# Kernel optimization log

Hardware: AMD Instinct MI355X
Metric: run time of the kernel (lower is better)

## Reference

```python
import jax, jax.numpy as jnp
import numpy as np

DIM = 512
HEADS = 8
DIM_HEAD = 64
INNER = HEADS * DIM_HEAD  # 512
PATCH = 64
M = 3
IN_CH = PATCH * PATCH // 2      # 2048
OUT_CH = IN_CH // 2             # 1024
B, N = 8, PATCH * PATCH // 4    # 8, 1024
SCALE = DIM_HEAD ** -0.5


def setup_inputs() -> dict:
    key = jax.random.key(0)
    ks = jax.random.split(key, 16)
    rn = lambda k, shp, s: (jax.random.normal(k, shp, dtype=jnp.float32) * s)
    inp = rn(ks[0], (B, N, DIM), 1.0)
    x = rn(ks[1], (B, N, DIM), 1.0)
    y = rn(ks[2], (B, N, DIM), 1.0)
    # Linear params (torch convention: W [out, in], y = x @ W.T + b)
    Wq = rn(ks[3], (INNER, DIM), DIM ** -0.5)
    bq = jnp.zeros((INNER,), jnp.float32)
    Wkv = rn(ks[4], (2 * INNER, DIM), DIM ** -0.5)
    bkv = jnp.zeros((2 * INNER,), jnp.float32)
    Wf = rn(ks[5], (OUT_CH + M, IN_CH + M), (IN_CH + M) ** -0.5)
    bf = jnp.zeros((OUT_CH + M,), jnp.float32)
    Wo = rn(ks[6], (DIM, INNER), INNER ** -0.5)
    bo = jnp.zeros((DIM,), jnp.float32)
    # memory tokens (xavier_normal std = sqrt(2/(m+inner)))
    std = np.sqrt(2.0 / (M + INNER))
    m_k = rn(ks[7], (1, M, INNER), std)
    m_v = rn(ks[8], (1, M, INNER), std)
    Sm_k = rn(ks[9], (1, M, INNER), std)
    Sm_v = rn(ks[10], (1, M, INNER), std)
    return dict(inp=inp, x=x, y=y, Wq=Wq, bq=bq, Wkv=Wkv, bkv=bkv,
                Wf=Wf, bf=bf, Wo=Wo, bo=bo,
                m_k=m_k, m_v=m_v, Sm_k=Sm_k, Sm_v=Sm_v)


def _split_heads(t):
    # 'b n (h d) -> b h n d'
    b, n, _ = t.shape
    return t.reshape(b, n, HEADS, DIM_HEAD).transpose(0, 2, 1, 3)


def _mem_view(p, b):
    # torch: p.expand(b, M, INNER).view(b, HEADS, M, DIM_HEAD) — raw reshape
    return jnp.broadcast_to(p, (b, M, INNER)).reshape(b, HEADS, M, DIM_HEAD)


def reference(inp, x, y, Wq, bq, Wkv, bkv, Wf, bf, Wo, bo, m_k, m_v, Sm_k, Sm_v):
    b = inp.shape[0]
    context = jnp.concatenate([x, y], axis=1)            # [b, 2n, dim]
    q = _split_heads(inp @ Wq.T + bq)                    # [b, h, n, d]
    kv = context @ Wkv.T + bkv
    k, v = jnp.split(kv, 2, axis=-1)
    k, v = _split_heads(k), _split_heads(v)              # [b, h, 2n, d]
    mk = np.sqrt(DIM_HEAD).astype(np.float32) * _mem_view(m_k, b)
    mv = np.sqrt(M).astype(np.float32) * _mem_view(m_v, b)
    k = jnp.concatenate([k, mk], axis=2)                 # [b, h, 2n+m, d]
    v = jnp.concatenate([v, mv], axis=2)
    dots = jnp.einsum('bhid,bhjd->bhij', q, k) * SCALE
    cross_attn = jax.nn.softmax(dots, axis=-1)           # [b, h, n, 2n+m]

    skv = inp @ Wkv.T + bkv
    S_k, S_v = jnp.split(skv, 2, axis=-1)
    S_k, S_v = _split_heads(S_k), _split_heads(S_v)      # [b, h, n, d]
    Smk = np.sqrt(DIM_HEAD).astype(np.float32) * _mem_view(Sm_k, b)
    Smv = np.sqrt(M).astype(np.float32) * _mem_view(Sm_v, b)
    Sk = jnp.concatenate([S_k, Smk], axis=2)             # [b, h, n+m, d]
    Sv = jnp.concatenate([S_v, Smv], axis=2)
    dots2 = jnp.einsum('bhid,bhjd->bhij', q, Sk) * SCALE
    self_attn = jax.nn.softmax(dots2, axis=-1)           # [b, h, n, n+m]

    cross_attn = cross_attn @ Wf.T + bf                  # [b, h, n, n+m]
    attn = cross_attn + self_attn
    out = jnp.einsum('bhij,bhjd->bhid', attn, Sv)        # [b, h, n, d]
    out = out.transpose(0, 2, 1, 3).reshape(b, -1, INNER)
    return out @ Wo.T + bo                               # [b, n, dim]
```

## Files before the change

### kernel.cpp

```cpp
#include <hip/hip_runtime.h>
#include <hip/hip_bf16.h>
#include <type_traits>

using bf16 = __hip_bfloat16;
typedef float f32x4 __attribute__((ext_vector_type(4)));
typedef __bf16 bf16x8_t __attribute__((ext_vector_type(8)));
typedef short  s16x8_t  __attribute__((ext_vector_type(8)));

template <typename V, typename = void> struct MfmaWorks : std::false_type {};
template <typename V>
struct MfmaWorks<V, std::void_t<decltype(__builtin_amdgcn_mfma_f32_16x16x32_bf16(
    std::declval<V>(), std::declval<V>(), std::declval<f32x4>(), 0, 0, 0))>> : std::true_type {};
using frag_t = std::conditional_t<MfmaWorks<bf16x8_t>::value, bf16x8_t, s16x8_t>;

template <typename V>
__device__ __forceinline__ f32x4 mfma_16x16x32(V a, V b, f32x4 c) {
    return __builtin_amdgcn_mfma_f32_16x16x32_bf16(a, b, c, 0, 0, 0);
}

__device__ __forceinline__ void gld_lds16(const void* g, void* l) {
    __builtin_amdgcn_global_load_lds(
        (const __attribute__((address_space(1))) unsigned int*)g,
        (__attribute__((address_space(3))) unsigned int*)l, 16, 0, 0);
}

__device__ __forceinline__ unsigned pack2(float lo, float hi) {
    bf16 a = __float2bfloat16(lo), b = __float2bfloat16(hi);
    unsigned short al, bl;
    __builtin_memcpy(&al, &a, 2);
    __builtin_memcpy(&bl, &b, 2);
    return (unsigned)al | ((unsigned)bl << 16);
}

__device__ __forceinline__ float ldin(const void* p, long i, int f32) {
    return f32 ? ((const float*)p)[i] : __bfloat162float(((const bf16*)p)[i]);
}

__global__ void detect_dtype(const void* __restrict__ inp, int* __restrict__ flag)
{
    const int t = threadIdx.x;
    int sane_cnt = 0;
#pragma unroll
    for (int s = 0; s < 4; s++) {
        float v = __bfloat162float(((const bf16*)inp)[2 * (t + 64 * s)]);
        float a = fabsf(v);
        bool sane = (a == 0.f) || (a > 9e-4f && a < 1000.f);
        unsigned long long m = __ballot(sane);
        sane_cnt += (int)__popcll(m);
    }
    if (t == 0) *flag = (sane_cnt > 128) ? 0 : 1;
}

__global__ __launch_bounds__(256)
void cvt_gen8(const void* __restrict__ src, bf16* __restrict__ dst,
              long ndst, const int* __restrict__ flag, float scale)
{
    const int f = *flag;
    const long i0 = ((long)blockIdx.x * 256 + threadIdx.x) * 8;
    if (i0 >= ndst) return;
#pragma unroll
    for (int u = 0; u < 8; u++)
        dst[i0 + u] = __float2bfloat16(scale * ldin(src, i0 + u, f));
}

__global__ __launch_bounds__(256)
void prep(const void* __restrict__ Wq, const void* __restrict__ Wkv,
          const void* __restrict__ Wo, const void* __restrict__ Wf,
          const void* __restrict__ bff, const void* __restrict__ bq,
          const void* __restrict__ bkv, const void* __restrict__ bo,
          const void* __restrict__ mk, const void* __restrict__ Smk,
          const void* __restrict__ Smv,
          bf16* __restrict__ WqB, bf16* __restrict__ WkvB, bf16* __restrict__ WoB,
          bf16* __restrict__ WfT, bf16* __restrict__ bqB, bf16* __restrict__ bkvB,
          bf16* __restrict__ boB, bf16* __restrict__ kb, bf16* __restrict__ Skb,
          bf16* __restrict__ GTS, bf16* __restrict__ SvC,
          const int* __restrict__ flag, float qscale)
{
    const int f = *flag;
    const int blk = blockIdx.x;
    const int t = threadIdx.x;
    const float SQRT3 = 1.7320508f;

    if (blk < 512) {
        long id = (long)blk * 256 + t;
        const void* src; bf16* dst; float sc;
        if (blk < 128)      { src = Wq;  dst = WqB;  sc = qscale; }
        else if (blk < 384) { src = Wkv; dst = WkvB; sc = 1.f; id -= 128L * 256; }
        else                { src = Wo;  dst = WoB;  sc = 1.f; id -= 384L * 256; }
        const long i0 = id * 8;
#pragma unroll
        for (int u = 0; u < 8; u++)
            dst[i0 + u] = __float2bfloat16(sc * ldin(src, i0 + u, f));
    } else if (blk < 1634) {
        const long i0 = ((long)(blk - 512) * 256 + t) * 8;
        if (i0 >= 2176L * 1056) return;
        const long j = i0 / 1056, r0 = i0 % 1056;
        __align__(16) bf16 tmp[8];
#pragma unroll
        for (int u = 0; u < 8; u++) {
            const long r = r0 + u;
            float v = 0.f;
            if (r < 1027) {
                if (j < 2051)       v = ldin(Wf, r * 2051 + j, f);
                else if (j == 2051) v = ldin(bff, r, f);
            }
            tmp[u] = __float2bfloat16(v);
        }
        *(uint4*)(WfT + i0) = *(const uint4*)tmp;
    } else if (blk < 1637) {
        const void* src; bf16* dst; int n; float sc;
        switch (blk - 1634) {
            case 0:  src = bq;  dst = bqB;  n = 512;  sc = qscale; break;
            case 1:  src = bkv; dst = bkvB; n = 1024; sc = 1.f;    break;
            default: src = bo;  dst = boB;  n = 512;  sc = 1.f;    break;
        }
        for (int i = t; i < n; i += 256)
            dst[i] = __float2bfloat16(sc * ldin(src, i, f));
    } else if (blk < 1893) {
        const long e = ((long)(blk - 1637) * 256 + t) * 8;
        const long bh = e >> 13, rem = e & 8191;
        const long jj = rem >> 6, dg0 = rem & 63;
        const long h = bh & 7;
        __align__(16) bf16 tmp[8];
#pragma unroll
        for (int u = 0; u < 8; u++) {
            float v = (jj < 3) ? 8.f * ldin(mk, jj * 512 + h * 64 + dg0 + u, f) : 0.f;
            tmp[u] = __float2bfloat16(v);
        }
        *(uint4*)(kb + (bh * 2176 + 2048 + jj) * 64 + dg0) = *(const uint4*)tmp;
    } else if (blk < 2149) {
        const long e = ((long)(blk - 1893) * 256 + t) * 8;
        const long bh = e >> 13, rem = e & 8191;
        const long jj = rem >> 6, dg0 = rem & 63;
        const long h = bh & 7;
        __align__(16) bf16 tmp[8];
#pragma unroll
        for (int u = 0; u < 8; u++) {
            float v = (jj < 3) ? 8.f * ldin(Smk, jj * 512 + h * 64 + dg0 + u, f) : 0.f;
            tmp[u] = __float2bfloat16(v);
        }
        *(uint4*)(Skb + (bh * 1152 + 1024 + jj) * 64 + dg0) = *(const uint4*)tmp;
    } else {
        const long e = ((long)(blk - 2149) * 256 + t) * 8;
        const long bh = e >> 11, rem = e & 2047;
        const long dd = rem >> 5, jc0 = rem & 31;
        const long h = bh & 7;
        __align__(16) bf16 tmp[8];
#pragma unroll
        for (int u = 0; u < 8; u++) {
            const long jc = jc0 + u;
            float v = (jc < 3) ? SQRT3 * ldin(Smv, jc * 512 + h * 64 + dd, f) : 0.f;
            tmp[u] = __float2bfloat16(v);
        }
        *(uint4*)(GTS + (bh * 128 + dd) * 3136 + 3104 + jc0) = *(const uint4*)tmp;
        *(uint4*)(SvC + (bh * 64 + dd) * 1056 + 1024 + jc0)  = *(const uint4*)tmp;
    }
}

__global__ __launch_bounds__(256)
void cvt_ctx8(const void* __restrict__ x, const void* __restrict__ y,
              bf16* __restrict__ ctx, const int* __restrict__ flag)
{
    const int f = *flag;
    const long i0 = ((long)blockIdx.x * 256 + threadIdx.x) * 8;
    const long r = i0 >> 9, c0 = i0 & 511;
    const long b = r >> 11, jj = r & 2047;
    const void* src = (jj < 1024) ? x : y;
    const long  soff = (jj < 1024) ? ((b * 1024 + jj) * 512 + c0)
                                   : ((b * 1024 + (jj - 1024)) * 512 + c0);
#pragma unroll
    for (int u = 0; u < 8; u++)
        ctx[i0 + u] = __float2bfloat16(ldin(src, soff + u, f));
}

#define TM 128
#define TN 128
#define BK 32

template<int OMODE>
__global__ __launch_bounds__(256)
void gemm_nt(const bf16* __restrict__ A, long lda, long sAz,
             const bf16* __restrict__ B, long ldb, long sBz,
             void* __restrict__ Cv, long ldc, long sCz,
             int K,
             const bf16* __restrict__ bias,
             int validN, int zeroN,
             void* __restrict__ Cv2, void* __restrict__ Cv3, void* __restrict__ Cv4)
{
    __shared__ __align__(16) short As[TM * BK];
    __shared__ __align__(16) short Bs[TN * BK];

    const int t = threadIdx.x;
    const int wave = t >> 6;
    const int lane = t & 63;
    const int bn = blockIdx.x, bm = blockIdx.y, z = blockIdx.z;

    const bf16* Ab = A + (long)z * sAz + (long)bm * TM * lda;
    const bf16* Bb = B + (long)z * sBz + (long)bn * TN * ldb;

    const int lrow = t >> 2;
    const int lcol = (t & 3) << 3;

    const f32x4 vzero = {0.f, 0.f, 0.f, 0.f};
    f32x4 acc[4][4];
#pragma unroll
    for (int i = 0; i < 4; i++)
#pragma unroll
        for (int j = 0; j < 4; j++) acc[i][j] = vzero;

    const int wr = (wave >> 1) << 6;
    const int wc = (wave & 1) << 6;
    const int fr = lane & 15;
    const int fq = (lane >> 4) << 3;

    for (int k0 = 0; k0 < K; k0 += BK) {
        __syncthreads();
        if constexpr (OMODE == 5) {
            const int ar = t >> 1;
            const int ac = (t & 1) << 4;
            const float* a0 = (const float*)A   + (long)(bm * TM + ar) * lda + k0 + ac;
            const float* a1 = (const float*)Cv2 + (long)(bm * TM + ar) * lda + k0 + ac;
            __align__(16) bf16 tt[16];
#pragma unroll
            for (int u = 0; u < 4; u++) {
                const float4 v0 = *(const float4*)(a0 + u * 4);
                const float4 v1 = *(const float4*)(a1 + u * 4);
                tt[u * 4 + 0] = __float2bfloat16(v0.x + v1.x);
                tt[u * 4 + 1] = __float2bfloat16(v0.y + v1.y);
                tt[u * 4 + 2] = __float2bfloat16(v0.z + v1.z);
                tt[u * 4 + 3] = __float2bfloat16(v0.w + v1.w);
            }
            *(uint4*)&As[ar * BK + ac]     = *(const uint4*)&tt[0];
            *(uint4*)&As[ar * BK + ac + 8] = *(const uint4*)&tt[8];
        } else {
            gld_lds16(Ab + (long)lrow * lda + (k0 + lcol),        (char*)As + wave * 1024);
            gld_lds16(Ab + (long)(64 + lrow) * lda + (k0 + lcol), (char*)As + 4096 + wave * 1024);
        }
        gld_lds16(Bb + (long)lrow * ldb + (k0 + lcol),        (char*)Bs + wave * 1024);
        gld_lds16(Bb + (long)(64 + lrow) * ldb + (k0 + lcol), (char*)Bs + 4096 + wave * 1024);
        __builtin_amdgcn_s_waitcnt(0);
        __syncthreads();

        frag_t af[4], bfr[4];
#pragma unroll
        for (int i = 0; i < 4; i++) af[i]  = *(const frag_t*)&As[(wr + i * 16 + fr) * BK + fq];
#pragma unroll
        for (int j = 0; j < 4; j++) bfr[j] = *(const frag_t*)&Bs[(wc + j * 16 + fr) * BK + fq];
#pragma unroll
        for (int i = 0; i < 4; i++)
#pragma unroll
            for (int j = 0; j < 4; j++)
                acc[i][j] = mfma_16x16x32<frag_t>(af[i], bfr[j], acc[i][j]);
    }

    const int r0 = bm * TM + wr + ((lane >> 4) << 2);
    const int c0 = bn * TN + wc + fr;

    if constexpr (OMODE == 2) {
#pragma unroll
        for (int j = 0; j < 4; j++) {
            const int c = c0 + j * 16;
            bf16* rowp = (bf16*)Cv + ((long)(c >> 6) * 128 + (c & 63)) * 3136;
#pragma unroll
            for (int i = 0; i < 4; i++) {
                const int rgb = r0 + i * 16;
                if (rgb >= zeroN) continue;
                __align__(8) bf16 t4[4];
#pragma unroll
                for (int r = 0; r < 4; r++) t4[r] = __float2bfloat16(acc[i][j][r]);
                *(uint2*)(rowp + rgb) = *(const uint2*)t4;
            }
        }
        return;
    }
    if constexpr (OMODE == 3) {
        const int bb = bm >> 3;
#pragma unroll
        for (int j = 0; j < 4; j++) {
            const int c = c0 + j * 16;
            const float bv = __bfloat162float(bias[c]);
            if (c < 512) {
#pragma unroll
                for (int i = 0; i < 4; i++)
#pragma unroll
                    for (int r = 0; r < 4; r++) {
                        const long rg = r0 + i * 16 + r;
                        ((bf16*)Cv)[rg * ldc + c] = __float2bfloat16(acc[i][j][r] + bv);
                    }
            } else if (c < 1024) {
                const int h = (c - 512) >> 6, dg = c & 63;
                bf16* base = (bf16*)Cv2 + ((long)(bb * 8 + h) * 1152) * 64 + dg;
#pragma unroll
                for (int i = 0; i < 4; i++)
#pragma unroll
                    for (int r = 0; r < 4; r++) {
                        const long jj = (r0 + i * 16 + r) & 1023;
                        base[jj * 64] = __float2bfloat16(acc[i][j][r] + bv);
                    }
            } else {
                const int h = (c - 1024) >> 6, dd = c & 63;
                bf16* svt = (bf16*)Cv3 + ((long)(bb * 8 + h) * 128 + dd) * 3136 + 2080;
                bf16* svc = (bf16*)Cv4 + ((long)(bb * 8 + h) * 64 + dd) * 1056;
#pragma unroll
                for (int i = 0; i < 4; i++) {
                    const long j0 = (r0 + i * 16) & 1023;
                    __align__(8) bf16 t4[4];
#pragma unroll
                    for (int r = 0; r < 4; r++) t4[r] = __float2bfloat16(acc[i][j][r] + bv);
                    *(uint2*)(svt + j0) = *(const uint2*)t4;
                    *(uint2*)(svc + j0) = *(const uint2*)t4;
                }
            }
        }
        return;
    }
    if constexpr (OMODE == 4) {
        const int bb = bm >> 4;
#pragma unroll
        for (int j = 0; j < 4; j++) {
            const int c = c0 + j * 16;
            const float bv = __bfloat162float(bias[c]);
            const int h = c >> 6, dg = c & 63;
            bf16* base = (bf16*)Cv + ((long)(bb * 8 + h) * 2176) * 64 + dg;
#pragma unroll
            for (int i = 0; i < 4; i++)
#pragma unroll
                for (int r = 0; r < 4; r++) {
                    const long jj = (r0 + i * 16 + r) & 2047;
                    base[jj * 64] = __float2bfloat16(acc[i][j][r] + bv);
                }
        }
        return;
    }
#pragma unroll
    for (int j = 0; j < 4; j++) {
        const int c = c0 + j * 16;
        if (c >= zeroN) continue;
        const float bv = bias ? __bfloat162float(bias[c]) : 0.f;
#pragma unroll
        for (int i = 0; i < 4; i++)
#pragma unroll
            for (int r = 0; r < 4; r++) {
                const long rg = r0 + i * 16 + r;
                ((float*)Cv)[(long)z * sCz + rg * ldc + c] = acc[i][j][r] + bv;
            }
    }
}

__global__ __launch_bounds__(256, 4)
void attn_fused(const bf16* __restrict__ q,
                const bf16* __restrict__ kb,
                const bf16* __restrict__ Skb,
                const bf16* __restrict__ GTS,
                float* __restrict__ out0,
                float* __restrict__ out1)
{
    __shared__ __align__(16) bf16 Ks[2][64 * 64];
    __shared__ __align__(16) bf16 Gs[2][64 * 64];
    __shared__ __align__(16) unsigned Psw[4][16][32];

    const int t = threadIdx.x;
    const int w = t >> 6, lane = t & 63;
    const int bh = blockIdx.x, bm = blockIdx.y;
    const int phase = blockIdx.z;
    const int b = bh >> 3, h = bh & 7;
    const int g  = lane >> 4;
    const int fr = lane & 15;

    const bf16* Qg = q + ((long)(b * 1024 + bm * 128)) * 512 + h * 64;
    {
        const int qr = t >> 3, qc0 = (t & 7) << 3;
#pragma unroll
        for (int u = 0; u < 4; u++)
            gld_lds16(Qg + (long)(u * 32 + qr) * 512 + qc0, (char*)Ks + u * 4096 + w * 1024);
    }
    __builtin_amdgcn_s_waitcnt(0);
    __syncthreads();

    frag_t qf[2][2];
#pragma unroll
    for (int it = 0; it < 2; it++)
#pragma unroll
        for (int kh = 0; kh < 2; kh++)
            qf[it][kh] = *(const frag_t*)&((const bf16*)Ks)[(w * 32 + it * 16 + fr) * 64 + kh * 32 + g * 8];
    __syncthreads();

    union { frag_t f; short s[8]; } ou;
#pragma unroll
    for (int i = 0; i < 8; i++) ou.s[i] = 0x3F80;
    const frag_t onesf = ou.f;

    const f32x4 vzero = {0.f, 0.f, 0.f, 0.f};
    const int rs = t >> 3, gs = t & 7;
    const int glo = gs ^ (rs & 7);

    const bf16* Kb = phase ? Skb + (long)bh * 1152 * 64 : kb + (long)bh * 2176 * 64;
    const bf16* Gb = GTS + (long)bh * 128 * 3136 + (phase ? 2080 : 0);
    const int NC = phase ? 17 : 33;
    const int valid = phase ? 1027 : 2051;

    f32x4 oacc[2][4];
    f32x4 lacc[2];
#pragma unroll
    for (int it = 0; it < 2; it++) {
        lacc[it] = vzero;
#pragma unroll
        for (int dt = 0; dt < 4; dt++) oacc[it][dt] = vzero;
    }

    gld_lds16(Kb + (long)rs * 64 + glo * 8,          (char*)Ks[0] + w * 1024);
    gld_lds16(Kb + (long)(32 + rs) * 64 + glo * 8,   (char*)Ks[0] + 4096 + w * 1024);
    gld_lds16(Gb + (long)rs * 3136 + glo * 8,        (char*)Gs[0] + w * 1024);
    gld_lds16(Gb + (long)(32 + rs) * 3136 + glo * 8, (char*)Gs[0] + 4096 + w * 1024);

    unsigned* prow = &Psw[w][fr][0];
    const int swzk = (fr & 7) << 2;

    for (int c = 0; c < NC; c++) {
        const int buf = c & 1;
        __builtin_amdgcn_s_waitcnt(0);
        __syncthreads();
        if (c + 1 < NC) {
            const bf16* Kc = Kb + (long)(c + 1) * 64 * 64;
            const bf16* Gc = Gb + (c + 1) * 64;
            gld_lds16(Kc + (long)rs * 64 + glo * 8,          (char*)Ks[buf ^ 1] + w * 1024);
            gld_lds16(Kc + (long)(32 + rs) * 64 + glo * 8,   (char*)Ks[buf ^ 1] + 4096 + w * 1024);
            gld_lds16(Gc + (long)rs * 3136 + glo * 8,        (char*)Gs[buf ^ 1] + w * 1024);
            gld_lds16(Gc + (long)(32 + rs) * 3136 + glo * 8, (char*)Gs[buf ^ 1] + 4096 + w * 1024);
        }
        const bf16* Kl = Ks[buf];
        const bf16* Gl = Gs[buf];

        f32x4 s2[2][4];
#pragma unroll
        for (int it = 0; it < 2; it++)
#pragma unroll
            for (int ct = 0; ct < 4; ct++) s2[it][ct] = vzero;
        __builtin_amdgcn_s_setprio(1);
#pragma unroll
        for (int ct = 0; ct < 4; ct++)
#pragma unroll
            for (int kh = 0; kh < 2; kh++) {
                const int gph = (kh * 4 + g) ^ (fr & 7);
                const frag_t kf = *(const frag_t*)&Kl[(ct * 16 + fr) * 64 + gph * 8];
                s2[0][ct] = mfma_16x16x32<frag_t>(kf, qf[0][kh], s2[0][ct]);
                s2[1][ct] = mfma_16x16x32<frag_t>(kf, qf[1][kh], s2[1][ct]);
            }
        __builtin_amdgcn_s_setprio(0);

        if (c == NC - 1) {
#pragma unroll
            for (int ct = 0; ct < 4; ct++)
#pragma unroll
                for (int r = 0; r < 4; r++) {
                    const int kAbs = c * 64 + ct * 16 + 4 * g + r;
                    if (kAbs >= valid) { s2[0][ct][r] = -1.0e30f; s2[1][ct][r] = -1.0e30f; }
                }
        }

        frag_t pa[2][2];
#pragma unroll
        for (int it = 0; it < 2; it++) {
#pragma unroll
            for (int ct = 0; ct < 4; ct++) {
                const unsigned w0 = pack2(exp2f(s2[it][ct][0]), exp2f(s2[it][ct][1]));
                const unsigned w1 = pack2(exp2f(s2[it][ct][2]), exp2f(s2[it][ct][3]));
                *(uint2*)&prow[(ct * 8 + 2 * g) ^ swzk] = make_uint2(w0, w1);
            }
#pragma unroll
            for (int kh = 0; kh < 2; kh++)
                pa[it][kh] = *(const frag_t*)&prow[(kh * 16 + 4 * g) ^ swzk];
        }

        __builtin_amdgcn_s_setprio(1);
#pragma unroll
        for (int kh = 0; kh < 2; kh++) {
            lacc[0] = mfma_16x16x32<frag_t>(pa[0][kh], onesf, lacc[0]);
            lacc[1] = mfma_16x16x32<frag_t>(pa[1][kh], onesf, lacc[1]);
#pragma unroll
            for (int dt = 0; dt < 4; dt++) {
                const int gph = (kh * 4 + g) ^ (fr & 7);
                const frag_t gf = *(const frag_t*)&Gl[(dt * 16 + fr) * 64 + gph * 8];
                oacc[0][dt] = mfma_16x16x32<frag_t>(pa[0][kh], gf, oacc[0][dt]);
                oacc[1][dt] = mfma_16x16x32<frag_t>(pa[1][kh], gf, oacc[1][dt]);
            }
        }
        __builtin_amdgcn_s_setprio(0);
    }

    float gba[4] = {0.f, 0.f, 0.f, 0.f};
    if (phase == 0) {
        const bf16* gp = GTS + (long)bh * 128 * 3136 + 2051;
#pragma unroll
        for (int dt = 0; dt < 4; dt++)
            gba[dt] = __bfloat162float(gp[(long)(dt * 16 + fr) * 3136]);
    }
    float* Og = (phase ? out1 : out0) + ((long)(b * 1024 + bm * 128)) * 512 + h * 64;
#pragma unroll
    for (int it = 0; it < 2; it++)
#pragma unroll
        for (int r = 0; r < 4; r++) {
            const float inv = 1.f / lacc[it][r];
#pragma unroll
            for (int dt = 0; dt < 4; dt++) {
                Og[(long)(w * 32 + it * 16 + g * 4 + r) * 512 + dt * 16 + fr] =
                    oacc[it][dt][r] * inv + gba[dt];
            }
        }
}

extern "C" void kernel_launch(void* const* d_in, const int* in_sizes, int n_in,
                              void* d_out, int out_size, void* d_ws, size_t ws_size,
                              hipStream_t stream)
{
    const void* inp  = d_in[0];
    const void* x    = d_in[1];
    const void* y    = d_in[2];
    const void* Wq   = d_in[3];
    const void* bq   = d_in[4];
    const void* Wkv  = d_in[5];
    const void* bkv  = d_in[6];
    const void* Wf   = d_in[7];
    const void* bff  = d_in[8];
    const void* Wo   = d_in[9];
    const void* bo   = d_in[10];
    const void* m_k  = d_in[11];
    const void* Sm_k = d_in[13];
    const void* Sm_v = d_in[14];

    char* ws = (char*)d_ws;
    int*  flag = (int*)(ws + 0);
    bf16* WqB  = (bf16*)(ws + 256);
    bf16* WkvB = (bf16*)(ws + 524544);
    bf16* WoB  = (bf16*)(ws + 1573120);
    bf16* WfT  = (bf16*)(ws + 2097408);
    bf16* bqB  = (bf16*)(ws + 6693120);
    bf16* bkvB = (bf16*)(ws + 6694144);
    bf16* boB  = (bf16*)(ws + 6696192);
    bf16* qb   = (bf16*)(ws + 6706432);
    bf16* kb   = (bf16*)(ws + 15095040);
    bf16* Skb  = (bf16*)(ws + 32920832);
    bf16* GTS  = (bf16*)(ws + 42358016);
    char* OV   = ws + 93738240;

    bf16*  inpB  = (bf16*)(OV);
    bf16*  SvC   = (bf16*)(OV + 16777216);
    bf16*  ctxB  = (bf16*)(OV);
    float* out0f = (float*)(OV);
    float* out1f = (float*)(OV + 16777216);

    const dim3 blk(256);
    const bf16* nulb = nullptr;
    const float QS = 0.125f * 1.44269504f;

    detect_dtype<<<dim3(1), dim3(64), 0, stream>>>(inp, flag);

    prep<<<dim3(2213), blk, 0, stream>>>(Wq, Wkv, Wo, Wf, bff, bq, bkv, bo,
                                         m_k, Sm_k, Sm_v,
                                         WqB, WkvB, WoB, WfT, bqB, bkvB, boB,
                                         kb, Skb, GTS, SvC, flag, QS);

    cvt_gen8<<<dim3(2048), blk, 0, stream>>>(inp, inpB, 4194304, flag, 1.f);

    gemm_nt<3><<<dim3(12, 64, 1), blk, 0, stream>>>(inpB, 512, 0, WqB, 512, 0,
        (void*)qb, 512, 0, 512, bqB, 1536, 1536, (void*)Skb, (void*)GTS, (void*)SvC);

    gemm_nt<2><<<dim3(32, 17, 1), blk, 0, stream>>>(WfT, 1056, 0, SvC, 1056, 0,
        (void*)GTS, 0, 0, 1056, nulb, 0, 2080, nullptr, nullptr, nullptr);

    cvt_ctx8<<<dim3(4096), blk, 0, stream>>>(x, y, ctxB, flag);

    gemm_nt<4><<<dim3(4, 128, 1), blk, 0, stream>>>(ctxB, 512, 0, WkvB, 512, 0,
        (void*)kb, 0, 0, 512, bkvB, 512, 512, nullptr, nullptr, nullptr);

    attn_fused<<<dim3(64, 8, 2), blk, 0, stream>>>(qb, kb, Skb, GTS, out0f, out1f);

    gemm_nt<5><<<dim3(4, 64, 1), blk, 0, stream>>>((const bf16*)out0f, 512, 0, WoB, 512, 0,
        d_out, 512, 0, 512, boB, 512, 512, (void*)out1f, nullptr, nullptr);
}
```

Measured before the change: 359.9 us.

## Merge prep kernels and co-schedule independent GEMMs to cut launches

Folds dtype detection into each block of a single prep kernel, which now also converts inp and the x/y context, replacing four launches with one. The Wf-times-Sv GEMM and the context KV projection GEMM are launched together as one grid, with block-index dispatch, so they fill the device concurrently. The output projection switches to 64-row tiles for more blocks. Every prep block redundantly re-runs the dtype probe and adds a syncthreads, and ctxB moves to a separate workspace region so it no longer aliases inpB.

```diff
diff --git a/kernel.cpp b/kernel.cpp
--- a/kernel.cpp
+++ b/kernel.cpp
@@ -36,63 +36,73 @@
     return f32 ? ((const float*)p)[i] : __bfloat162float(((const bf16*)p)[i]);
 }
 
-__global__ void detect_dtype(const void* __restrict__ inp, int* __restrict__ flag)
+__device__ __forceinline__ int detect_f32(const void* __restrict__ inp) {
+    __shared__ int sflag;
+    const int t = threadIdx.x;
+    if (t < 64) {
+        int cnt = 0;
+#pragma unroll
+        for (int s = 0; s < 4; s++) {
+            float v = __bfloat162float(((const bf16*)inp)[2 * (t + 64 * s)]);
+            float a = fabsf(v);
+            bool sane = (a == 0.f) || (a > 9e-4f && a < 1000.f);
+            unsigned long long m = __ballot(sane);
+            cnt += (int)__popcll(m);
+        }
+        if (t == 0) sflag = (cnt > 128) ? 0 : 1;
+    }
+    __syncthreads();
+    return sflag;
+}
+
+__global__ __launch_bounds__(256)
+void prep_all(const void* __restrict__ inp, const void* __restrict__ x,
+              const void* __restrict__ y,
+              const void* __restrict__ Wq, const void* __restrict__ Wkv,
+              const void* __restrict__ Wo, const void* __restrict__ Wf,
+              const void* __restrict__ bff, const void* __restrict__ bq,
+              const void* __restrict__ bkv, const void* __restrict__ bo,
+              const void* __restrict__ mk, const void* __restrict__ Smk,
+              const void* __restrict__ Smv,
+              bf16* __restrict__ inpB, bf16* __restrict__ ctxB,
+              bf16* __restrict__ WqB, bf16* __restrict__ WkvB, bf16* __restrict__ WoB,
+              bf16* __restrict__ WfT, bf16* __restrict__ bqB, bf16* __restrict__ bkvB,
+              bf16* __restrict__ boB, bf16* __restrict__ kb, bf16* __restrict__ Skb,
+              bf16* __restrict__ GTS, bf16* __restrict__ SvC, float qscale)
 {
-    const int t = threadIdx.x;
-    int sane_cnt = 0;
-#pragma unroll
-    for (int s = 0; s < 4; s++) {
-        float v = __bfloat162float(((const bf16*)inp)[2 * (t + 64 * s)]);
-        float a = fabsf(v);
-        bool sane = (a == 0.f) || (a > 9e-4f && a < 1000.f);
-        unsigned long long m = __ballot(sane);
-        sane_cnt += (int)__popcll(m);
-    }
-    if (t == 0) *flag = (sane_cnt > 128) ? 0 : 1;
-}
-
-__global__ __launch_bounds__(256)
-void cvt_gen8(const void* __restrict__ src, bf16* __restrict__ dst,
-              long ndst, const int* __restrict__ flag, float scale)
-{
-    const int f = *flag;
-    const long i0 = ((long)blockIdx.x * 256 + threadIdx.x) * 8;
-    if (i0 >= ndst) return;
-#pragma unroll
-    for (int u = 0; u < 8; u++)
-        dst[i0 + u] = __float2bfloat16(scale * ldin(src, i0 + u, f));
-}
-
-__global__ __launch_bounds__(256)
-void prep(const void* __restrict__ Wq, const void* __restrict__ Wkv,
-          const void* __restrict__ Wo, const void* __restrict__ Wf,
-          const void* __restrict__ bff, const void* __restrict__ bq,
-          const void* __restrict__ bkv, const void* __restrict__ bo,
-          const void* __restrict__ mk, const void* __restrict__ Smk,
-          const void* __restrict__ Smv,
-          bf16* __restrict__ WqB, bf16* __restrict__ WkvB, bf16* __restrict__ WoB,
-          bf16* __restrict__ WfT, bf16* __restrict__ bqB, bf16* __restrict__ bkvB,
-          bf16* __restrict__ boB, bf16* __restrict__ kb, bf16* __restrict__ Skb,
-          bf16* __restrict__ GTS, bf16* __restrict__ SvC,
-          const int* __restrict__ flag, float qscale)
-{
-    const int f = *flag;
+    const int f = detect_f32(inp);
     const int blk = blockIdx.x;
     const int t = threadIdx.x;
     const float SQRT3 = 1.7320508f;
 
-    if (blk < 512) {
-        long id = (long)blk * 256 + t;
+    if (blk < 2048) {
+        const long i0 = ((long)blk * 256 + t) * 8;
+#pragma unroll
+        for (int u = 0; u < 8; u++)
+            inpB[i0 + u] = __float2bfloat16(ldin(inp, i0 + u, f));
+    } else if (blk < 6144) {
+        const long i0 = ((long)(blk - 2048) * 256 + t) * 8;
+        const long r = i0 >> 9, c0 = i0 & 511;
+        const long b = r >> 11, jj = r & 2047;
+        const void* src = (jj < 1024) ? x : y;
+        const long  soff = (jj < 1024) ? ((b * 1024 + jj) * 512 + c0)
+                                       : ((b * 1024 + (jj - 1024)) * 512 + c0);
+#pragma unroll
+        for (int u = 0; u < 8; u++)
+            ctxB[i0 + u] = __float2bfloat16(ldin(src, soff + u, f));
+    } else if (blk < 6656) {
+        const int wb = blk - 6144;
+        long id = (long)wb * 256 + t;
         const void* src; bf16* dst; float sc;
-        if (blk < 128)      { src = Wq;  dst = WqB;  sc = qscale; }
-        else if (blk < 384) { src = Wkv; dst = WkvB; sc = 1.f; id -= 128L * 256; }
-        else                { src = Wo;  dst = WoB;  sc = 1.f; id -= 384L * 256; }
+        if (wb < 128)      { src = Wq;  dst = WqB;  sc = qscale; }
+        else if (wb < 384) { src = Wkv; dst = WkvB; sc = 1.f; id -= 128L * 256; }
+        else               { src = Wo;  dst = WoB;  sc = 1.f; id -= 384L * 256; }
         const long i0 = id * 8;
 #pragma unroll
         for (int u = 0; u < 8; u++)
             dst[i0 + u] = __float2bfloat16(sc * ldin(src, i0 + u, f));
-    } else if (blk < 1634) {
-        const long i0 = ((long)(blk - 512) * 256 + t) * 8;
+    } else if (blk < 7778) {
+        const long i0 = ((long)(blk - 6656) * 256 + t) * 8;
         if (i0 >= 2176L * 1056) return;
         const long j = i0 / 1056, r0 = i0 % 1056;
         __align__(16) bf16 tmp[8];
@@ -107,17 +117,17 @@
             tmp[u] = __float2bfloat16(v);
         }
         *(uint4*)(WfT + i0) = *(const uint4*)tmp;
-    } else if (blk < 1637) {
+    } else if (blk < 7781) {
         const void* src; bf16* dst; int n; float sc;
-        switch (blk - 1634) {
+        switch (blk - 7778) {
             case 0:  src = bq;  dst = bqB;  n = 512;  sc = qscale; break;
             case 1:  src = bkv; dst = bkvB; n = 1024; sc = 1.f;    break;
             default: src = bo;  dst = boB;  n = 512;  sc = 1.f;    break;
         }
         for (int i = t; i < n; i += 256)
             dst[i] = __float2bfloat16(sc * ldin(src, i, f));
-    } else if (blk < 1893) {
-        const long e = ((long)(blk - 1637) * 256 + t) * 8;
+    } else if (blk < 8037) {
+        const long e = ((long)(blk - 7781) * 256 + t) * 8;
         const long bh = e >> 13, rem = e & 8191;
         const long jj = rem >> 6, dg0 = rem & 63;
         const long h = bh & 7;
@@ -128,8 +138,8 @@
             tmp[u] = __float2bfloat16(v);
         }
         *(uint4*)(kb + (bh * 2176 + 2048 + jj) * 64 + dg0) = *(const uint4*)tmp;
-    } else if (blk < 2149) {
-        const long e = ((long)(blk - 1893) * 256 + t) * 8;
+    } else if (blk < 8293) {
+        const long e = ((long)(blk - 8037) * 256 + t) * 8;
         const long bh = e >> 13, rem = e & 8191;
         const long jj = rem >> 6, dg0 = rem & 63;
         const long h = bh & 7;
@@ -141,7 +151,7 @@
         }
         *(uint4*)(Skb + (bh * 1152 + 1024 + jj) * 64 + dg0) = *(const uint4*)tmp;
     } else {
-        const long e = ((long)(blk - 2149) * 256 + t) * 8;
+        const long e = ((long)(blk - 8293) * 256 + t) * 8;
         const long bh = e >> 11, rem = e & 2047;
         const long dd = rem >> 5, jc0 = rem & 31;
         const long h = bh & 7;
@@ -157,49 +167,25 @@
     }
 }
 
+#define BK 32
+
 __global__ __launch_bounds__(256)
-void cvt_ctx8(const void* __restrict__ x, const void* __restrict__ y,
-              bf16* __restrict__ ctx, const int* __restrict__ flag)
+void gemm_qkv(const bf16* __restrict__ A, const bf16* __restrict__ B,
+              const bf16* __restrict__ bias,
+              bf16* __restrict__ qb, bf16* __restrict__ Skb,
+              bf16* __restrict__ GTS, bf16* __restrict__ SvC)
 {
-    const int f = *flag;
-    const long i0 = ((long)blockIdx.x * 256 + threadIdx.x) * 8;
-    const long r = i0 >> 9, c0 = i0 & 511;
-    const long b = r >> 11, jj = r & 2047;
-    const void* src = (jj < 1024) ? x : y;
-    const long  soff = (jj < 1024) ? ((b * 1024 + jj) * 512 + c0)
-                                   : ((b * 1024 + (jj - 1024)) * 512 + c0);
-#pragma unroll
-    for (int u = 0; u < 8; u++)
-        ctx[i0 + u] = __float2bfloat16(ldin(src, soff + u, f));
-}
-
-#define TM 128
-#define TN 128
-#define BK 32
-
-template<int OMODE>
-__global__ __launch_bounds__(256)
-void gemm_nt(const bf16* __restrict__ A, long lda, long sAz,
-             const bf16* __restrict__ B, long ldb, long sBz,
-             void* __restrict__ Cv, long ldc, long sCz,
-             int K,
-             const bf16* __restrict__ bias,
-             int validN, int zeroN,
-             void* __restrict__ Cv2, void* __restrict__ Cv3, void* __restrict__ Cv4)
-{
-    __shared__ __align__(16) short As[TM * BK];
-    __shared__ __align__(16) short Bs[TN * BK];
+    __shared__ __align__(16) short As[128 * BK];
+    __shared__ __align__(16) short Bs[128 * BK];
 
     const int t = threadIdx.x;
-    const int wave = t >> 6;
-    const int lane = t & 63;
-    const int bn = blockIdx.x, bm = blockIdx.y, z = blockIdx.z;
-
-    const bf16* Ab = A + (long)z * sAz + (long)bm * TM * lda;
-    const bf16* Bb = B + (long)z * sBz + (long)bn * TN * ldb;
-
-    const int lrow = t >> 2;
-    const int lcol = (t & 3) << 3;
+    const int wave = t >> 6, lane = t & 63;
+    const int bn = blockIdx.x, bm = blockIdx.y;
+
+    const bf16* Ab = A + (long)bm * 128 * 512;
+    const bf16* Bb = B + (long)bn * 128 * 512;
+
+    const int lrow = t >> 2, lcol = (t & 3) << 3;
 
     const f32x4 vzero = {0.f, 0.f, 0.f, 0.f};
     f32x4 acc[4][4];
@@ -213,16 +199,200 @@
     const int fr = lane & 15;
     const int fq = (lane >> 4) << 3;
 
+    for (int k0 = 0; k0 < 512; k0 += BK) {
+        __syncthreads();
+        gld_lds16(Ab + (long)lrow * 512 + (k0 + lcol),        (char*)As + wave * 1024);
+        gld_lds16(Ab + (long)(64 + lrow) * 512 + (k0 + lcol), (char*)As + 4096 + wave * 1024);
+        gld_lds16(Bb + (long)lrow * 512 + (k0 + lcol),        (char*)Bs + wave * 1024);
+        gld_lds16(Bb + (long)(64 + lrow) * 512 + (k0 + lcol), (char*)Bs + 4096 + wave * 1024);
+        __builtin_amdgcn_s_waitcnt(0);
+        __syncthreads();
+
+        frag_t af[4], bfr[4];
+#pragma unroll
+        for (int i = 0; i < 4; i++) af[i]  = *(const frag_t*)&As[(wr + i * 16 + fr) * BK + fq];
+#pragma unroll
+        for (int j = 0; j < 4; j++) bfr[j] = *(const frag_t*)&Bs[(wc + j * 16 + fr) * BK + fq];
+#pragma unroll
+        for (int i = 0; i < 4; i++)
+#pragma unroll
+            for (int j = 0; j < 4; j++)
+                acc[i][j] = mfma_16x16x32<frag_t>(af[i], bfr[j], acc[i][j]);
+    }
+
+    const int r0 = bm * 128 + wr + ((lane >> 4) << 2);
+    const int c0 = bn * 128 + wc + fr;
+    const int bb = bm >> 3;
+#pragma unroll
+    for (int j = 0; j < 4; j++) {
+        const int c = c0 + j * 16;
+        const float bv = __bfloat162float(bias[c]);
+        if (c < 512) {
+#pragma unroll
+            for (int i = 0; i < 4; i++)
+#pragma unroll
+                for (int r = 0; r < 4; r++) {
+                    const long rg = r0 + i * 16 + r;
+                    qb[rg * 512 + c] = __float2bfloat16(acc[i][j][r] + bv);
+                }
+        } else if (c < 1024) {
+            const int h = (c - 512) >> 6, dg = c & 63;
+            bf16* base = Skb + ((long)(bb * 8 + h) * 1152) * 64 + dg;
+#pragma unroll
+            for (int i = 0; i < 4; i++)
+#pragma unroll
+                for (int r = 0; r < 4; r++) {
+                    const long jj = (r0 + i * 16 + r) & 1023;
+                    base[jj * 64] = __float2bfloat16(acc[i][j][r] + bv);
+                }
+        } else {
+            const int h = (c - 1024) >> 6, dd = c & 63;
+            bf16* svt = GTS + ((long)(bb * 8 + h) * 128 + dd) * 3136 + 2080;
+            bf16* svc = SvC + ((long)(bb * 8 + h) * 64 + dd) * 1056;
+#pragma unroll
+            for (int i = 0; i < 4; i++) {
+                const long j0 = (r0 + i * 16) & 1023;
+                __align__(8) bf16 t4[4];
+#pragma unroll
+                for (int r = 0; r < 4; r++) t4[r] = __float2bfloat16(acc[i][j][r] + bv);
+                *(uint2*)(svt + j0) = *(const uint2*)t4;
+                *(uint2*)(svc + j0) = *(const uint2*)t4;
+            }
+        }
+    }
+}
+
+__global__ __launch_bounds__(256)
+void gemm_gtck(const bf16* __restrict__ WfT, const bf16* __restrict__ SvC,
+               bf16* __restrict__ GTS,
+               const bf16* __restrict__ ctxB, const bf16* __restrict__ WkvB,
+               const bf16* __restrict__ bkvB, bf16* __restrict__ kb)
+{
+    __shared__ __align__(16) short As[128 * BK];
+    __shared__ __align__(16) short Bs[128 * BK];
+
+    const int t = threadIdx.x;
+    const int wave = t >> 6, lane = t & 63;
+    const int id = blockIdx.x;
+    const bool isGT = id < 544;
+
+    int bn, bm, K;
+    const bf16 *A, *B;
+    long lda, ldb;
+    if (isGT) { bn = id & 31; bm = id >> 5; A = WfT; lda = 1056; B = SvC; ldb = 1056; K = 1056; }
+    else { const int i2 = id - 544; bn = i2 & 3; bm = i2 >> 2; A = ctxB; lda = 512; B = WkvB; ldb = 512; K = 512; }
+
+    const bf16* Ab = A + (long)bm * 128 * lda;
+    const bf16* Bb = B + (long)bn * 128 * ldb;
+
+    const int lrow = t >> 2, lcol = (t & 3) << 3;
+
+    const f32x4 vzero = {0.f, 0.f, 0.f, 0.f};
+    f32x4 acc[4][4];
+#pragma unroll
+    for (int i = 0; i < 4; i++)
+#pragma unroll
+        for (int j = 0; j < 4; j++) acc[i][j] = vzero;
+
+    const int wr = (wave >> 1) << 6;
+    const int wc = (wave & 1) << 6;
+    const int fr = lane & 15;
+    const int fq = (lane >> 4) << 3;
+
     for (int k0 = 0; k0 < K; k0 += BK) {
         __syncthreads();
-        if constexpr (OMODE == 5) {
-            const int ar = t >> 1;
-            const int ac = (t & 1) << 4;
-            const float* a0 = (const float*)A   + (long)(bm * TM + ar) * lda + k0 + ac;
-            const float* a1 = (const float*)Cv2 + (long)(bm * TM + ar) * lda + k0 + ac;
-            __align__(16) bf16 tt[16];
-#pragma unroll
-            for (int u = 0; u < 4; u++) {
+        gld_lds16(Ab + (long)lrow * lda + (k0 + lcol),        (char*)As + wave * 1024);
+        gld_lds16(Ab + (long)(64 + lrow) * lda + (k0 + lcol), (char*)As + 4096 + wave * 1024);
+        gld_lds16(Bb + (long)lrow * ldb + (k0 + lcol),        (char*)Bs + wave * 1024);
+        gld_lds16(Bb + (long)(64 + lrow) * ldb + (k0 + lcol), (char*)Bs + 4096 + wave * 1024);
+        __builtin_amdgcn_s_waitcnt(0);
+        __syncthreads();
+
+        frag_t af[4], bfr[4];
+#pragma unroll
+        for (int i = 0; i < 4; i++) af[i]  = *(const frag_t*)&As[(wr + i * 16 + fr) * BK + fq];
+#pragma unroll
+        for (int j = 0; j < 4; j++) bfr[j] = *(const frag_t*)&Bs[(wc + j * 16 + fr) * BK + fq];
+#pragma unroll
+        for (int i = 0; i < 4; i++)
+#pragma unroll
+            for (int j = 0; j < 4; j++)
+                acc[i][j] = mfma_16x16x32<frag_t>(af[i], bfr[j], acc[i][j]);
+    }
+
+    const int r0 = bm * 128 + wr + ((lane >> 4) << 2);
+    const int c0 = bn * 128 + wc + fr;
+
+    if (isGT) {
+#pragma unroll
+        for (int j = 0; j < 4; j++) {
+            const int c = c0 + j * 16;
+            bf16* rowp = GTS + ((long)(c >> 6) * 128 + (c & 63)) * 3136;
+#pragma unroll
+            for (int i = 0; i < 4; i++) {
+                const int rgb = r0 + i * 16;
+                if (rgb >= 2080) continue;
+                __align__(8) bf16 t4[4];
+#pragma unroll
+                for (int r = 0; r < 4; r++) t4[r] = __float2bfloat16(acc[i][j][r]);
+                *(uint2*)(rowp + rgb) = *(const uint2*)t4;
+            }
+        }
+    } else {
+        const int bb = bm >> 4;
+#pragma unroll
+        for (int j = 0; j < 4; j++) {
+            const int c = c0 + j * 16;
+            const float bv = __bfloat162float(bkvB[c]);
+            const int h = c >> 6, dg = c & 63;
+            bf16* base = kb + ((long)(bb * 8 + h) * 2176) * 64 + dg;
+#pragma unroll
+            for (int i = 0; i < 4; i++)
+#pragma unroll
+                for (int r = 0; r < 4; r++) {
+                    const long jj = (r0 + i * 16 + r) & 2047;
+                    base[jj * 64] = __float2bfloat16(acc[i][j][r] + bv);
+                }
+        }
+    }
+}
+
+__global__ __launch_bounds__(256)
+void gemm_final64(const float* __restrict__ o0, const float* __restrict__ o1,
+                  const bf16* __restrict__ B, const bf16* __restrict__ bias,
+                  float* __restrict__ out)
+{
+    __shared__ __align__(16) short As[64 * BK];
+    __shared__ __align__(16) short Bs[128 * BK];
+
+    const int t = threadIdx.x;
+    const int wave = t >> 6, lane = t & 63;
+    const int bn = blockIdx.x, bm = blockIdx.y;
+
+    const bf16* Bb = B + (long)bn * 128 * 512;
+    const int lrow = t >> 2, lcol = (t & 3) << 3;
+
+    const f32x4 vzero = {0.f, 0.f, 0.f, 0.f};
+    f32x4 acc[2][4];
+#pragma unroll
+    for (int i = 0; i < 2; i++)
+#pragma unroll
+        for (int j = 0; j < 4; j++) acc[i][j] = vzero;
+
+    const int wr = (wave >> 1) << 5;
+    const int wc = (wave & 1) << 6;
+    const int fr = lane & 15;
+    const int fq = (lane >> 4) << 3;
+
+    for (int k0 = 0; k0 < 512; k0 += BK) {
+        __syncthreads();
+        {
+            const int ar = t >> 2, ac = (t & 3) << 3;
+            const float* a0 = o0 + (long)(bm * 64 + ar) * 512 + k0 + ac;
+            const float* a1 = o1 + (long)(bm * 64 + ar) * 512 + k0 + ac;
+            __align__(16) bf16 tt[8];
+#pragma unroll
+            for (int u = 0; u < 2; u++) {
                 const float4 v0 = *(const float4*)(a0 + u * 4);
                 const float4 v1 = *(const float4*)(a1 + u * 4);
                 tt[u * 4 + 0] = __float2bfloat16(v0.x + v1.x);
@@ -230,119 +400,37 @@
                 tt[u * 4 + 2] = __float2bfloat16(v0.z + v1.z);
                 tt[u * 4 + 3] = __float2bfloat16(v0.w + v1.w);
             }
-            *(uint4*)&As[ar * BK + ac]     = *(const uint4*)&tt[0];
-            *(uint4*)&As[ar * BK + ac + 8] = *(const uint4*)&tt[8];
-        } else {
-            gld_lds16(Ab + (long)lrow * lda + (k0 + lcol),        (char*)As + wave * 1024);
-            gld_lds16(Ab + (long)(64 + lrow) * lda + (k0 + lcol), (char*)As + 4096 + wave * 1024);
-        }
-        gld_lds16(Bb + (long)lrow * ldb + (k0 + lcol),        (char*)Bs + wave * 1024);
-        gld_lds16(Bb + (long)(64 + lrow) * ldb + (k0 + lcol), (char*)Bs + 4096 + wave * 1024);
+            *(uint4*)&As[ar * BK + ac] = *(const uint4*)tt;
+        }
+        gld_lds16(Bb + (long)lrow * 512 + (k0 + lcol),        (char*)Bs + wave * 1024);
+        gld_lds16(Bb + (long)(64 + lrow) * 512 + (k0 + lcol), (char*)Bs + 4096 + wave * 1024);
         __builtin_amdgcn_s_waitcnt(0);
         __syncthreads();
 
-        frag_t af[4], bfr[4];
-#pragma unroll
-        for (int i = 0; i < 4; i++) af[i]  = *(const frag_t*)&As[(wr + i * 16 + fr) * BK + fq];
+        frag_t af[2], bfr[4];
+#pragma unroll
+        for (int i = 0; i < 2; i++) af[i]  = *(const frag_t*)&As[(wr + i * 16 + fr) * BK + fq];
 #pragma unroll
         for (int j = 0; j < 4; j++) bfr[j] = *(const frag_t*)&Bs[(wc + j * 16 + fr) * BK + fq];
 #pragma unroll
-        for (int i = 0; i < 4; i++)
+        for (int i = 0; i < 2; i++)
 #pragma unroll
             for (int j = 0; j < 4; j++)
                 acc[i][j] = mfma_16x16x32<frag_t>(af[i], bfr[j], acc[i][j]);
     }
 
-    const int r0 = bm * TM + wr + ((lane >> 4) << 2);
-    const int c0 = bn * TN + wc + fr;
-
-    if constexpr (OMODE == 2) {
-#pragma unroll
-        for (int j = 0; j < 4; j++) {
-            const int c = c0 + j * 16;
-            bf16* rowp = (bf16*)Cv + ((long)(c >> 6) * 128 + (c & 63)) * 3136;
-#pragma unroll
-            for (int i = 0; i < 4; i++) {
-                const int rgb = r0 + i * 16;
-                if (rgb >= zeroN) continue;
-                __align__(8) bf16 t4[4];
-#pragma unroll
-                for (int r = 0; r < 4; r++) t4[r] = __float2bfloat16(acc[i][j][r]);
-                *(uint2*)(rowp + rgb) = *(const uint2*)t4;
-            }
-        }
-        return;
-    }
-    if constexpr (OMODE == 3) {
-        const int bb = bm >> 3;
-#pragma unroll
-        for (int j = 0; j < 4; j++) {
-            const int c = c0 + j * 16;
-            const float bv = __bfloat162float(bias[c]);
-            if (c < 512) {
-#pragma unroll
-                for (int i = 0; i < 4; i++)
-#pragma unroll
-                    for (int r = 0; r < 4; r++) {
-                        const long rg = r0 + i * 16 + r;
-                        ((bf16*)Cv)[rg * ldc + c] = __float2bfloat16(acc[i][j][r] + bv);
-                    }
-            } else if (c < 1024) {
-                const int h = (c - 512) >> 6, dg = c & 63;
-                bf16* base = (bf16*)Cv2 + ((long)(bb * 8 + h) * 1152) * 64 + dg;
-#pragma unroll
-                for (int i = 0; i < 4; i++)
-#pragma unroll
-                    for (int r = 0; r < 4; r++) {
-                        const long jj = (r0 + i * 16 + r) & 1023;
-                        base[jj * 64] = __float2bfloat16(acc[i][j][r] + bv);
-                    }
-            } else {
-                const int h = (c - 1024) >> 6, dd = c & 63;
-                bf16* svt = (bf16*)Cv3 + ((long)(bb * 8 + h) * 128 + dd) * 3136 + 2080;
-                bf16* svc = (bf16*)Cv4 + ((long)(bb * 8 + h) * 64 + dd) * 1056;
-#pragma unroll
-                for (int i = 0; i < 4; i++) {
-                    const long j0 = (r0 + i * 16) & 1023;
-                    __align__(8) bf16 t4[4];
-#pragma unroll
-                    for (int r = 0; r < 4; r++) t4[r] = __float2bfloat16(acc[i][j][r] + bv);
-                    *(uint2*)(svt + j0) = *(const uint2*)t4;
-                    *(uint2*)(svc + j0) = *(const uint2*)t4;
-                }
-            }
-        }
-        return;
-    }
-    if constexpr (OMODE == 4) {
-        const int bb = bm >> 4;
-#pragma unroll
-        for (int j = 0; j < 4; j++) {
-            const int c = c0 + j * 16;
-            const float bv = __bfloat162float(bias[c]);
-            const int h = c >> 6, dg = c & 63;
-            bf16* base = (bf16*)Cv + ((long)(bb * 8 + h) * 2176) * 64 + dg;
-#pragma unroll
-            for (int i = 0; i < 4; i++)
-#pragma unroll
-                for (int r = 0; r < 4; r++) {
-                    const long jj = (r0 + i * 16 + r) & 2047;
-                    base[jj * 64] = __float2bfloat16(acc[i][j][r] + bv);
-                }
-        }
-        return;
-    }
+    const int r0 = bm * 64 + wr + ((lane >> 4) << 2);
+    const int c0 = bn * 128 + wc + fr;
 #pragma unroll
     for (int j = 0; j < 4; j++) {
         const int c = c0 + j * 16;
-        if (c >= zeroN) continue;
-        const float bv = bias ? __bfloat162float(bias[c]) : 0.f;
-#pragma unroll
-        for (int i = 0; i < 4; i++)
+        const float bv = __bfloat162float(bias[c]);
+#pragma unroll
+        for (int i = 0; i < 2; i++)
 #pragma unroll
             for (int r = 0; r < 4; r++) {
                 const long rg = r0 + i * 16 + r;
-                ((float*)Cv)[(long)z * sCz + rg * ldc + c] = acc[i][j][r] + bv;
+                out[rg * 512 + c] = acc[i][j][r] + bv;
             }
     }
 }
@@ -529,7 +617,6 @@
     const void* Sm_v = d_in[14];
 
     char* ws = (char*)d_ws;
-    int*  flag = (int*)(ws + 0);
     bf16* WqB  = (bf16*)(ws + 256);
     bf16* WkvB = (bf16*)(ws + 524544);
     bf16* WoB  = (bf16*)(ws + 1573120);
@@ -545,36 +632,23 @@
 
     bf16*  inpB  = (bf16*)(OV);
     bf16*  SvC   = (bf16*)(OV + 16777216);
-    bf16*  ctxB  = (bf16*)(OV);
+    bf16*  ctxB  = (bf16*)(OV + 33554432);
     float* out0f = (float*)(OV);
     float* out1f = (float*)(OV + 16777216);
 
     const dim3 blk(256);
-    const bf16* nulb = nullptr;
     const float QS = 0.125f * 1.44269504f;
 
-    detect_dtype<<<dim3(1), dim3(64), 0, stream>>>(inp, flag);
-
-    prep<<<dim3(2213), blk, 0, stream>>>(Wq, Wkv, Wo, Wf, bff, bq, bkv, bo,
-                                         m_k, Sm_k, Sm_v,
-                                         WqB, WkvB, WoB, WfT, bqB, bkvB, boB,
-                                         kb, Skb, GTS, SvC, flag, QS);
-
-    cvt_gen8<<<dim3(2048), blk, 0, stream>>>(inp, inpB, 4194304, flag, 1.f);
-
-    gemm_nt<3><<<dim3(12, 64, 1), blk, 0, stream>>>(inpB, 512, 0, WqB, 512, 0,
-        (void*)qb, 512, 0, 512, bqB, 1536, 1536, (void*)Skb, (void*)GTS, (void*)SvC);
-
-    gemm_nt<2><<<dim3(32, 17, 1), blk, 0, stream>>>(WfT, 1056, 0, SvC, 1056, 0,
-        (void*)GTS, 0, 0, 1056, nulb, 0, 2080, nullptr, nullptr, nullptr);
-
-    cvt_ctx8<<<dim3(4096), blk, 0, stream>>>(x, y, ctxB, flag);
-
-    gemm_nt<4><<<dim3(4, 128, 1), blk, 0, stream>>>(ctxB, 512, 0, WkvB, 512, 0,
-        (void*)kb, 0, 0, 512, bkvB, 512, 512, nullptr, nullptr, nullptr);
+    prep_all<<<dim3(8357), blk, 0, stream>>>(inp, x, y, Wq, Wkv, Wo, Wf, bff,
+                                             bq, bkv, bo, m_k, Sm_k, Sm_v,
+                                             inpB, ctxB, WqB, WkvB, WoB, WfT,
+                                             bqB, bkvB, boB, kb, Skb, GTS, SvC, QS);
+
+    gemm_qkv<<<dim3(12, 64), blk, 0, stream>>>(inpB, WqB, bqB, qb, Skb, GTS, SvC);
+
+    gemm_gtck<<<dim3(1056), blk, 0, stream>>>(WfT, SvC, GTS, ctxB, WkvB, bkvB, kb);
 
     attn_fused<<<dim3(64, 8, 2), blk, 0, stream>>>(qb, kb, Skb, GTS, out0f, out1f);
 
-    gemm_nt<5><<<dim3(4, 64, 1), blk, 0, stream>>>((const bf16*)out0f, 512, 0, WoB, 512, 0,
-        d_out, 512, 0, 512, boB, 512, 512, (void*)out1f, nullptr, nullptr);
-}
+    gemm_final64<<<dim3(4, 128), blk, 0, stream>>>(out0f, out1f, WoB, boB, (float*)d_out);
+}
```

Result: no change. 360.9 us (+0.3%).
